# Optimization experiments

Hardware: AMD Instinct MI355X
Metric: run time of the kernel (lower is better)

Reference implementation:

```python
import jax, jax.numpy as jnp
import numpy as np

EPS = 1e-5  # BatchNorm1d default eps
NUM_HEADS = 8


def repbn(x, alpha, gamma, beta, rm, rv):
    # eval-mode RepBN over the channel (last) dim: BN(running stats) + alpha * x
    bn = (x - rm) * (gamma / jnp.sqrt(rv + EPS)) + beta
    return bn + alpha * x


def _forward(x, W_qkv, b_qkv, W_proj, b_proj, W1, b1, W2, b2, sa_w, sa_b,
             alpha1, gamma1, beta1, rm1, rv1, alpha2, gamma2, beta2, rm2, rv2):
    B, C, H, W = x.shape
    N = H * W
    D = C // NUM_HEADS
    t = x.reshape(B, C, N).transpose(0, 2, 1)  # [B, N, C]
    # --- FlashAttention (manual MHSA) ---
    qkv = (t @ W_qkv + b_qkv).reshape(B, N, 3, NUM_HEADS, D)
    q = qkv[:, :, 0].transpose(0, 2, 1, 3)  # [B, h, N, D]
    k = qkv[:, :, 1].transpose(0, 2, 1, 3)
    v = qkv[:, :, 2].transpose(0, 2, 1, 3)
    attn = jax.nn.softmax(jnp.einsum('bhnd,bhmd->bhnm', q, k) * (D ** -0.5), axis=-1)
    o = jnp.einsum('bhnm,bhmd->bhnd', attn, v).transpose(0, 2, 1, 3).reshape(B, N, C)
    o = o @ W_proj + b_proj
    # residual + blended norm (eval -> RepBN)
    t = repbn(t + o, alpha1, gamma1, beta1, rm1, rv1)
    # --- FFN with SpatialSILU activation ---
    h = t @ W1 + b1  # [B, N, cm]
    # depthwise 1x1 conv over the batch dim (channels==B per original unsqueeze(0))
    wgt = sa_w[:, None, None] * h + sa_b[:, None, None]
    h = h * jax.nn.sigmoid(wgt * h)
    f = h @ W2 + b2
    t = repbn(t + f, alpha2, gamma2, beta2, rm2, rv2)
    return t.transpose(0, 2, 1).reshape(B, C, H, W)


def setup_inputs() -> dict:
    key = jax.random.key(0)
    ks = jax.random.split(key, 8)
    B, C, H, W = 256, 256, 14, 14
    cm = 2048
    s = 0.02
    f32 = jnp.float32
    return {
        'x': jax.random.normal(ks[0], (B, C, H, W), f32),
        'W_qkv': jax.random.normal(ks[1], (C, 3 * C), f32) * s,
        'b_qkv': jnp.zeros((3 * C,), f32),
        'W_proj': jax.random.normal(ks[2], (C, C), f32) * s,
        'b_proj': jnp.zeros((C,), f32),
        'W1': jax.random.normal(ks[3], (C, cm), f32) * s,
        'b1': jnp.zeros((cm,), f32),
        'W2': jax.random.normal(ks[4], (cm, C), f32) * s,
        'b2': jnp.zeros((C,), f32),
        'sa_w': jax.random.normal(ks[5], (B,), f32) * s,
        'sa_b': jnp.zeros((B,), f32),
        'alpha1': jnp.ones((), f32),
        'gamma1': jnp.ones((C,), f32),
        'beta1': jnp.zeros((C,), f32),
        'rm1': jax.random.normal(ks[6], (C,), f32) * 0.1,
        'rv1': jnp.ones((C,), f32),
        'alpha2': jnp.ones((), f32),
        'gamma2': jnp.ones((C,), f32),
        'beta2': jnp.zeros((C,), f32),
        'rm2': jax.random.normal(ks[7], (C,), f32) * 0.1,
        'rv2': jnp.ones((C,), f32),
    }


def reference(x, W_qkv, b_qkv, W_proj, b_proj, W1, b1, W2, b2, sa_w, sa_b,
              alpha1, gamma1, beta1, rm1, rv1, alpha2, gamma2, beta2, rm2, rv2):
    return _forward(x, W_qkv, b_qkv, W_proj, b_proj, W1, b1, W2, b2, sa_w, sa_b,
                    alpha1, gamma1, beta1, rm1, rv1, alpha2, gamma2, beta2, rm2, rv2)
```

## Files before the change

kernel.cpp:

```cpp
#include <hip/hip_runtime.h>

using u16 = unsigned short;

typedef __bf16 bf16x8 __attribute__((ext_vector_type(8)));
typedef u16    u16x8  __attribute__((ext_vector_type(8)));
typedef float  f32x4  __attribute__((ext_vector_type(4)));

__device__ __forceinline__ float b2f(u16 u) {
    union { unsigned int i; float f; } c; c.i = ((unsigned int)u) << 16; return c.f;
}
__device__ __forceinline__ u16 f2b(float f) {
    union { float f; unsigned int i; } c; c.f = f;
    unsigned int i = c.i;
    return (u16)((i + 0x7FFFu + ((i >> 16) & 1u)) >> 16);
}
__device__ __forceinline__ float u2f(unsigned int u) {
    union { unsigned int i; float f; } c; c.i = u; return c.f;
}

#define AS1 __attribute__((address_space(1)))
#define AS3 __attribute__((address_space(3)))
__device__ __forceinline__ void glds16(const u16* g, u16* l) {
    __builtin_amdgcn_global_load_lds((const AS1 void*)(const void*)g,
                                     (AS3 void*)(void*)l, 16, 0, 0);
}

__global__ void btrans_f2b(const float* __restrict__ in, u16* __restrict__ out, int R, int C) {
    __shared__ u16 tile[32][33];
    const int c0 = blockIdx.x * 32, r0 = blockIdx.y * 32;
    const size_t base = (size_t)blockIdx.z * R * C;
    const int tx = threadIdx.x, ty = threadIdx.y;
    #pragma unroll
    for (int i = ty; i < 32; i += 8) {
        int r = r0 + i, c = c0 + tx;
        tile[i][tx] = (r < R && c < C) ? f2b(in[base + (size_t)r * C + c]) : (u16)0;
    }
    __syncthreads();
    #pragma unroll
    for (int i = ty; i < 32; i += 8) {
        int c = c0 + i, r = r0 + tx;
        if (c < C && r < R) out[base + (size_t)c * R + r] = tile[tx][i];
    }
}

__global__ void btrans_b2f(const u16* __restrict__ in, float* __restrict__ out, int R, int C) {
    __shared__ u16 tile[32][33];
    const int c0 = blockIdx.x * 32, r0 = blockIdx.y * 32;
    const size_t base = (size_t)blockIdx.z * R * C;
    const int tx = threadIdx.x, ty = threadIdx.y;
    #pragma unroll
    for (int i = ty; i < 32; i += 8) {
        int r = r0 + i, c = c0 + tx;
        tile[i][tx] = (r < R && c < C) ? in[base + (size_t)r * C + c] : (u16)0;
    }
    __syncthreads();
    #pragma unroll
    for (int i = ty; i < 32; i += 8) {
        int c = c0 + i, r = r0 + tx;
        if (c < C && r < R) out[base + (size_t)c * R + r] = b2f(tile[tx][i]);
    }
}

template<int EPI>
__launch_bounds__(512, 4)
__global__ void gemm_bt(const u16* __restrict__ A, const u16* __restrict__ BT,
                        const float* __restrict__ bias, u16* __restrict__ C,
                        int M, int N, int K, int row0,
                        const u16* __restrict__ R0,
                        const float* __restrict__ g, const float* __restrict__ be,
                        const float* __restrict__ rmv, const float* __restrict__ rvv,
                        const float* __restrict__ alpha,
                        const float* __restrict__ saw, const float* __restrict__ sab) {
    __shared__ __align__(16) u16 SL[16384];
    const int tid  = threadIdx.x;
    const int wave = tid >> 6, lane = tid & 63;
    const int wm = wave >> 2, wn = wave & 3;
    const int quad = lane >> 4, l16 = lane & 15;

    const unsigned gx = gridDim.x;
    unsigned lin = blockIdx.y * gx + blockIdx.x;
    const unsigned nwg = gx * gridDim.y;
    const unsigned q8 = nwg >> 3, r8 = nwg & 7;
    const unsigned xcd = lin & 7, loc = lin >> 3;
    lin = (xcd < r8 ? xcd * (q8 + 1) : r8 * (q8 + 1) + (xcd - r8) * q8) + loc;
    const int m0 = (int)(lin / gx) * 128, n0 = (int)(lin % gx) * 128;

    const int srow = lane >> 2;
    const int scol = (((lane & 3) ^ ((srow >> 1) & 3)) * 8);
    const size_t aoff = (size_t)(m0 + wave * 16 + srow) * K + scol;
    const size_t boff = (size_t)(n0 + wave * 16 + srow) * K + scol;
    u16* aS = SL + wave * 512;
    u16* bS = SL + 8192 + wave * 512;

    const int cfrag = (quad ^ ((l16 >> 1) & 3)) * 8;

    f32x4 acc[4][2] = {};
    const int niter = K >> 5;

    auto stage = [&](int buf, size_t kn) {
        const int bo = buf * 4096;
        glds16(A  + aoff + kn, aS + bo);
        glds16(BT + boff + kn, bS + bo);
    };

    auto kstep = [&](int cur, int kt) {
        __syncthreads();
        if (kt + 1 < niter) stage(cur ^ 1, (size_t)(kt + 1) << 5);
        const u16* ab = SL + cur * 4096;
        const u16* bb = SL + 8192 + cur * 4096;
        bf16x8 af[4], bfr[2];
        #pragma unroll
        for (int i = 0; i < 4; i++)
            af[i] = *(const bf16x8*)&ab[(wm * 64 + i * 16 + l16) * 32 + cfrag];
        #pragma unroll
        for (int j = 0; j < 2; j++)
            bfr[j] = *(const bf16x8*)&bb[(wn * 32 + j * 16 + l16) * 32 + cfrag];
        #pragma unroll
        for (int i = 0; i < 4; i++)
            #pragma unroll
            for (int j = 0; j < 2; j++)
                acc[i][j] = __builtin_amdgcn_mfma_f32_16x16x32_bf16(af[i], bfr[j], acc[i][j], 0, 0, 0);
    };

    stage(0, 0);
    int kt = 0;
    for (; kt + 2 <= niter; kt += 2) { kstep(0, kt); kstep(1, kt + 1); }
    if (kt < niter) kstep(kt & 1, kt);

    __syncthreads();

    float alphav = 0.f;
    if (EPI == 1) alphav = alpha[0];

    if (EPI == 1) {
        #pragma unroll
        for (int c = tid; c < 2048; c += 512) {
            int row = c >> 4, colc = (c & 15) * 8;
            *(u16x8*)&SL[row * 128 + colc] =
                *(const u16x8*)&R0[(size_t)(m0 + row) * N + n0 + colc];
        }
        __syncthreads();
    }

    float biasv[2], k0v[2], k1v[2];
    #pragma unroll
    for (int j = 0; j < 2; j++) {
        const int col = n0 + wn * 32 + j * 16 + l16;
        biasv[j] = bias[col];
        if (EPI == 1) {
            float sc = g[col] * rsqrtf(rvv[col] + 1e-5f);
            k1v[j] = sc + alphav;
            k0v[j] = be[col] - rmv[col] * sc;
        }
    }

    const int dup = l16 & 1;
    const int pr  = l16 >> 1;
    u16* Crow = C + (size_t)(m0 + wm * 64 + quad * 4 + 2 * dup) * N
                  + (n0 + wn * 32 + pr * 2);

    #pragma unroll
    for (int i = 0; i < 4; i++) {
        #pragma unroll
        for (int j = 0; j < 2; j++) {
            float vv[4];
            #pragma unroll
            for (int r = 0; r < 4; r++) {
                float v = acc[i][j][r] + biasv[j];
                if (EPI == 1) {
                    const int rowL = wm * 64 + i * 16 + quad * 4 + r;
                    const int colp = wn * 32 + j * 16 + (l16 & ~1);
                    unsigned rd = *(const unsigned*)&SL[rowL * 128 + colp];
                    unsigned fb = dup ? (rd & 0xffff0000u) : (rd << 16);
                    float x = v + u2f(fb);
                    v = fmaf(x, k1v[j], k0v[j]);
                } else if (EPI == 2) {
                    const int row = row0 + m0 + wm * 64 + i * 16 + quad * 4 + r;
                    const int bidx = row / 196;
                    float w = fmaf(saw[bidx], v, sab[bidx]);
                    v = v / (1.f + __expf(-w * v));
                }
                vv[r] = v;
            }
            unsigned D[4];
            #pragma unroll
            for (int r = 0; r < 4; r++) {
                float o  = __shfl_xor(vv[r], 1, 64);
                float lo = dup ? o : vv[r];
                float hi = dup ? vv[r] : o;
                unsigned d;
                asm("v_cvt_pk_bf16_f32 %0, %1, %2" : "=v"(d) : "v"(lo), "v"(hi));
                D[r] = d;
            }
            unsigned s0 = dup ? D[2] : D[0];
            unsigned s1 = dup ? D[3] : D[1];
            u16* p = Crow + (size_t)i * 16 * N + j * 16;
            *(unsigned*)p       = s0;
            *(unsigned*)(p + N) = s1;
        }
    }
}

__launch_bounds__(256)
__global__ void attn_kernel(const u16* __restrict__ qkv, u16* __restrict__ o) {
    __shared__ __align__(16) u16 Kb[224 * 32];
    __shared__ __align__(16) u16 Vt[32 * 232];
    __shared__ __align__(16) u16 Pl[4][16 * 232];
    const int tid  = threadIdx.x;
    const int wave = tid >> 6, lane = tid & 63;
    const int quad = lane >> 4, l16 = lane & 15;
    const int b = blockIdx.x >> 3, h = blockIdx.x & 7;
    const u16* qg = qkv + (size_t)b * 196 * 768 + h * 32;
    const float scale = 0.17677669529663687f;

    for (int idx = tid; idx < 896; idx += 256) {
        int row = idx >> 2, dp = (idx & 3) * 8;
        u16x8 kv = {};
        if (row < 196) kv = *(const u16x8*)&qg[(size_t)row * 768 + 256 + dp];
        *(u16x8*)&Kb[row * 32 + dp] = kv;
    }
    for (int idx = tid; idx < 224 * 32; idx += 256) {
        int row = idx >> 5, d = idx & 31;
        Vt[d * 232 + row] = (row < 196) ? qg[(size_t)row * 768 + 512 + d] : (u16)0;
    }
    for (int c = lane; c < 16 * 24; c += 64) {
        int m = c / 24, cc = 208 + (c % 24);
        Pl[wave][m * 232 + cc] = 0;
    }
    __syncthreads();

    for (int t = wave; t < 13; t += 4) {
        const int m0 = t * 16;
        bf16x8 aq = {};
        const int qrow = m0 + l16;
        if (qrow < 196) aq = *(const bf16x8*)&qg[(size_t)qrow * 768 + quad * 8];

        f32x4 s[13];
        #pragma unroll
        for (int ct = 0; ct < 13; ct++) {
            bf16x8 bk = *(const bf16x8*)&Kb[(ct * 16 + l16) * 32 + quad * 8];
            s[ct] = __builtin_amdgcn_mfma_f32_16x16x32_bf16(aq, bk, (f32x4){0.f, 0.f, 0.f, 0.f}, 0, 0, 0);
        }
        if (l16 >= 4) {
            #pragma unroll
            for (int r = 0; r < 4; r++) s[12][r] = -1e30f;
        }
        float mx[4] = {-1e30f, -1e30f, -1e30f, -1e30f};
        #pragma unroll
        for (int ct = 0; ct < 13; ct++)
            #pragma unroll
            for (int r = 0; r < 4; r++) mx[r] = fmaxf(mx[r], s[ct][r]);
        #pragma unroll
        for (int off = 1; off < 16; off <<= 1)
            #pragma unroll
            for (int r = 0; r < 4; r++) mx[r] = fmaxf(mx[r], __shfl_xor(mx[r], off, 64));
        float sum[4] = {0.f, 0.f, 0.f, 0.f};
        #pragma unroll
        for (int ct = 0; ct < 13; ct++) {
            #pragma unroll
            for (int r = 0; r < 4; r++) {
                float p = __expf((s[ct][r] - mx[r]) * scale);
                sum[r] += p;
                Pl[wave][(quad * 4 + r) * 232 + ct * 16 + l16] = f2b(p);
            }
        }
        #pragma unroll
        for (int off = 1; off < 16; off <<= 1)
            #pragma unroll
            for (int r = 0; r < 4; r++) sum[r] += __shfl_xor(sum[r], off, 64);
        float inv[4];
        #pragma unroll
        for (int r = 0; r < 4; r++) inv[r] = 1.f / sum[r];

        #pragma unroll
        for (int nt = 0; nt < 2; nt++) {
            f32x4 ao = {0.f, 0.f, 0.f, 0.f};
            #pragma unroll
            for (int kc = 0; kc < 7; kc++) {
                bf16x8 ap = *(const bf16x8*)&Pl[wave][l16 * 232 + kc * 32 + quad * 8];
                bf16x8 bv = *(const bf16x8*)&Vt[(nt * 16 + l16) * 232 + kc * 32 + quad * 8];
                ao = __builtin_amdgcn_mfma_f32_16x16x32_bf16(ap, bv, ao, 0, 0, 0);
            }
            #pragma unroll
            for (int r = 0; r < 4; r++) {
                const int gm = m0 + quad * 4 + r;
                if (gm < 196)
                    o[((size_t)b * 196 + gm) * 256 + h * 32 + nt * 16 + l16] = f2b(ao[r] * inv[r]);
            }
        }
    }
}

extern "C" void kernel_launch(void* const* d_in, const int* in_sizes, int n_in,
                              void* d_out, int out_size, void* d_ws, size_t ws_size,
                              hipStream_t stream) {
    const float* x      = (const float*)d_in[0];
    const float* Wqkv   = (const float*)d_in[1];
    const float* bqkv   = (const float*)d_in[2];
    const float* Wproj  = (const float*)d_in[3];
    const float* bproj  = (const float*)d_in[4];
    const float* W1     = (const float*)d_in[5];
    const float* b1     = (const float*)d_in[6];
    const float* W2     = (const float*)d_in[7];
    const float* b2     = (const float*)d_in[8];
    const float* saw    = (const float*)d_in[9];
    const float* sab    = (const float*)d_in[10];
    const float* alpha1 = (const float*)d_in[11];
    const float* g1     = (const float*)d_in[12];
    const float* be1    = (const float*)d_in[13];
    const float* rm1    = (const float*)d_in[14];
    const float* rv1    = (const float*)d_in[15];
    const float* alpha2 = (const float*)d_in[16];
    const float* g2     = (const float*)d_in[17];
    const float* be2    = (const float*)d_in[18];
    const float* rm2    = (const float*)d_in[19];
    const float* rv2    = (const float*)d_in[20];

    const int B = 256, Cc = 256, Np = 196, CM = 2048;
    const int M = B * Np;

    auto al = [](size_t s) { return (s + 255) & ~(size_t)255; };
    char* ws = (char*)d_ws;
    const size_t o_t0  = 0;
    const size_t o_t1  = o_t0 + al((size_t)M * Cc * 2);
    const size_t o_wq  = o_t1 + al((size_t)M * Cc * 2);
    const size_t o_wp  = o_wq + al((size_t)768 * Cc * 2);
    const size_t o_w1  = o_wp + al((size_t)Cc * Cc * 2);
    const size_t o_w2  = o_w1 + al((size_t)Cc * CM * 2);
    const size_t o_scr = o_w2 + al((size_t)CM * Cc * 2);
    const size_t S = (ws_size > o_scr) ? ws_size - o_scr : 0;

    u16* t0     = (u16*)(ws + o_t0);
    u16* t1b    = (u16*)(ws + o_t1);
    u16* WqkvT  = (u16*)(ws + o_wq);
    u16* WprojT = (u16*)(ws + o_wp);
    u16* W1T    = (u16*)(ws + o_w1);
    u16* W2T    = (u16*)(ws + o_w2);
    u16* scr    = (u16*)(ws + o_scr);
    u16* t2     = t0;
    u16* obuf   = (u16*)d_out;
    float* out  = (float*)d_out;

    int nq = 1; while (nq < 8 && ((size_t)(M / nq) * 768 * 2) > S) nq *= 2;
    const int nf_opts[7] = {1, 2, 4, 8, 14, 28, 56};
    int nf = 56;
    for (int i = 0; i < 7; ++i) {
        if (((size_t)(M / nf_opts[i]) * CM * 2) <= S) { nf = nf_opts[i]; break; }
    }
    const int Mq = M / nq, Bq = B / nq;
    const int Mf = M / nf;

    dim3 tb(32, 8, 1);
    btrans_f2b<<<dim3((Np + 31) / 32, (Cc + 31) / 32, B), tb, 0, stream>>>(x, t0, Cc, Np);
    btrans_f2b<<<dim3(768 / 32, Cc / 32, 1), tb, 0, stream>>>(Wqkv,  WqkvT,  Cc, 768);
    btrans_f2b<<<dim3(Cc  / 32, Cc / 32, 1), tb, 0, stream>>>(Wproj, WprojT, Cc, Cc);
    btrans_f2b<<<dim3(CM  / 32, Cc / 32, 1), tb, 0, stream>>>(W1,    W1T,    Cc, CM);
    btrans_f2b<<<dim3(Cc  / 32, CM / 32, 1), tb, 0, stream>>>(W2,    W2T,    CM, Cc);

    for (int c = 0; c < nq; ++c) {
        gemm_bt<0><<<dim3(768 / 128, Mq / 128), 512, 0, stream>>>(
            t0 + (size_t)c * Mq * Cc, WqkvT, bqkv, scr, Mq, 768, Cc, 0,
            nullptr, nullptr, nullptr, nullptr, nullptr, nullptr, nullptr, nullptr);
        attn_kernel<<<dim3(Bq * 8), 256, 0, stream>>>(scr, obuf + (size_t)c * Mq * Cc);
    }

    gemm_bt<1><<<dim3(Cc / 128, M / 128), 512, 0, stream>>>(
        obuf, WprojT, bproj, t1b, M, Cc, Cc, 0,
        t0, g1, be1, rm1, rv1, alpha1, nullptr, nullptr);

    for (int c = 0; c < nf; ++c) {
        gemm_bt<2><<<dim3(CM / 128, Mf / 128), 512, 0, stream>>>(
            t1b + (size_t)c * Mf * Cc, W1T, b1, scr, Mf, CM, Cc, c * Mf,
            nullptr, nullptr, nullptr, nullptr, nullptr, nullptr, saw, sab);
        gemm_bt<1><<<dim3(Cc / 128, Mf / 128), 512, 0, stream>>>(
            scr, W2T, b2, t2 + (size_t)c * Mf * Cc, Mf, Cc, CM, 0,
            t1b + (size_t)c * Mf * Cc, g2, be2, rm2, rv2, alpha2, nullptr, nullptr);
    }

    btrans_b2f<<<dim3((Cc + 31) / 32, (Np + 31) / 32, B), tb, 0, stream>>>(t2, out, Np, Cc);
}
```

Measured before the change: 542.9 us.

## Enlarge GEMM block tile to 256x128 with 64x64 per-wave tiles

Changes the GEMM block tile from 128x128 to 256x128. The 8 waves are rearranged into a 4x2 grid, so each wave owns a 64x64 output tile and accumulates 4x4 MFMA fragments. The aim is more data reuse per LDS fragment load and less global traffic per output. In exchange the LDS footprint, accumulator register pressure and residual-epilogue complexity all grow: the residual is now staged in two halves with extra barriers. The grid shrinks to half as many blocks, and chunking options are trimmed so the row counts stay divisible by 256, which may reduce occupancy and parallelism.

```diff
diff --git a/kernel.cpp b/kernel.cpp
--- a/kernel.cpp
+++ b/kernel.cpp
@@ -71,10 +71,10 @@
                         const float* __restrict__ rmv, const float* __restrict__ rvv,
                         const float* __restrict__ alpha,
                         const float* __restrict__ saw, const float* __restrict__ sab) {
-    __shared__ __align__(16) u16 SL[16384];
+    __shared__ __align__(16) u16 SL[24576];
     const int tid  = threadIdx.x;
     const int wave = tid >> 6, lane = tid & 63;
-    const int wm = wave >> 2, wn = wave & 3;
+    const int wm = wave >> 1, wn = wave & 1;
     const int quad = lane >> 4, l16 = lane & 15;
 
     const unsigned gx = gridDim.x;
@@ -83,42 +83,41 @@
     const unsigned q8 = nwg >> 3, r8 = nwg & 7;
     const unsigned xcd = lin & 7, loc = lin >> 3;
     lin = (xcd < r8 ? xcd * (q8 + 1) : r8 * (q8 + 1) + (xcd - r8) * q8) + loc;
-    const int m0 = (int)(lin / gx) * 128, n0 = (int)(lin % gx) * 128;
+    const int m0 = (int)(lin / gx) * 256, n0 = (int)(lin % gx) * 128;
 
     const int srow = lane >> 2;
     const int scol = (((lane & 3) ^ ((srow >> 1) & 3)) * 8);
-    const size_t aoff = (size_t)(m0 + wave * 16 + srow) * K + scol;
-    const size_t boff = (size_t)(n0 + wave * 16 + srow) * K + scol;
-    u16* aS = SL + wave * 512;
-    u16* bS = SL + 8192 + wave * 512;
+    const size_t aoff0 = (size_t)(m0 + wave * 32 + srow) * K + scol;
+    const size_t aoff1 = aoff0 + (size_t)16 * K;
+    const size_t boff  = (size_t)(n0 + wave * 16 + srow) * K + scol;
 
     const int cfrag = (quad ^ ((l16 >> 1) & 3)) * 8;
 
-    f32x4 acc[4][2] = {};
+    f32x4 acc[4][4] = {};
     const int niter = K >> 5;
 
     auto stage = [&](int buf, size_t kn) {
-        const int bo = buf * 4096;
-        glds16(A  + aoff + kn, aS + bo);
-        glds16(BT + boff + kn, bS + bo);
+        glds16(A  + aoff0 + kn, SL + buf * 8192 + wave * 1024);
+        glds16(A  + aoff1 + kn, SL + buf * 8192 + wave * 1024 + 512);
+        glds16(BT + boff  + kn, SL + 16384 + buf * 4096 + wave * 512);
     };
 
     auto kstep = [&](int cur, int kt) {
         __syncthreads();
         if (kt + 1 < niter) stage(cur ^ 1, (size_t)(kt + 1) << 5);
-        const u16* ab = SL + cur * 4096;
-        const u16* bb = SL + 8192 + cur * 4096;
-        bf16x8 af[4], bfr[2];
+        const u16* ab = SL + cur * 8192;
+        const u16* bb = SL + 16384 + cur * 4096;
+        bf16x8 af[4], bfr[4];
         #pragma unroll
         for (int i = 0; i < 4; i++)
             af[i] = *(const bf16x8*)&ab[(wm * 64 + i * 16 + l16) * 32 + cfrag];
         #pragma unroll
-        for (int j = 0; j < 2; j++)
-            bfr[j] = *(const bf16x8*)&bb[(wn * 32 + j * 16 + l16) * 32 + cfrag];
+        for (int j = 0; j < 4; j++)
+            bfr[j] = *(const bf16x8*)&bb[(wn * 64 + j * 16 + l16) * 32 + cfrag];
         #pragma unroll
         for (int i = 0; i < 4; i++)
             #pragma unroll
-            for (int j = 0; j < 2; j++)
+            for (int j = 0; j < 4; j++)
                 acc[i][j] = __builtin_amdgcn_mfma_f32_16x16x32_bf16(af[i], bfr[j], acc[i][j], 0, 0, 0);
     };
 
@@ -132,20 +131,10 @@
     float alphav = 0.f;
     if (EPI == 1) alphav = alpha[0];
 
-    if (EPI == 1) {
-        #pragma unroll
-        for (int c = tid; c < 2048; c += 512) {
-            int row = c >> 4, colc = (c & 15) * 8;
-            *(u16x8*)&SL[row * 128 + colc] =
-                *(const u16x8*)&R0[(size_t)(m0 + row) * N + n0 + colc];
-        }
-        __syncthreads();
-    }
-
-    float biasv[2], k0v[2], k1v[2];
-    #pragma unroll
-    for (int j = 0; j < 2; j++) {
-        const int col = n0 + wn * 32 + j * 16 + l16;
+    float biasv[4], k0v[4], k1v[4];
+    #pragma unroll
+    for (int j = 0; j < 4; j++) {
+        const int col = n0 + wn * 64 + j * 16 + l16;
         biasv[j] = bias[col];
         if (EPI == 1) {
             float sc = g[col] * rsqrtf(rvv[col] + 1e-5f);
@@ -157,47 +146,72 @@
     const int dup = l16 & 1;
     const int pr  = l16 >> 1;
     u16* Crow = C + (size_t)(m0 + wm * 64 + quad * 4 + 2 * dup) * N
-                  + (n0 + wn * 32 + pr * 2);
-
-    #pragma unroll
-    for (int i = 0; i < 4; i++) {
-        #pragma unroll
-        for (int j = 0; j < 2; j++) {
-            float vv[4];
-            #pragma unroll
-            for (int r = 0; r < 4; r++) {
-                float v = acc[i][j][r] + biasv[j];
-                if (EPI == 1) {
-                    const int rowL = wm * 64 + i * 16 + quad * 4 + r;
-                    const int colp = wn * 32 + j * 16 + (l16 & ~1);
-                    unsigned rd = *(const unsigned*)&SL[rowL * 128 + colp];
-                    unsigned fb = dup ? (rd & 0xffff0000u) : (rd << 16);
-                    float x = v + u2f(fb);
-                    v = fmaf(x, k1v[j], k0v[j]);
-                } else if (EPI == 2) {
+                  + (n0 + wn * 64 + pr * 2);
+
+    auto emit = [&]() {
+        #pragma unroll
+        for (int i = 0; i < 4; i++) {
+            float swv4[4], sbv4[4];
+            if (EPI == 2) {
+                #pragma unroll
+                for (int r = 0; r < 4; r++) {
                     const int row = row0 + m0 + wm * 64 + i * 16 + quad * 4 + r;
                     const int bidx = row / 196;
-                    float w = fmaf(saw[bidx], v, sab[bidx]);
-                    v = v / (1.f + __expf(-w * v));
+                    swv4[r] = saw[bidx]; sbv4[r] = sab[bidx];
                 }
-                vv[r] = v;
-            }
-            unsigned D[4];
-            #pragma unroll
-            for (int r = 0; r < 4; r++) {
-                float o  = __shfl_xor(vv[r], 1, 64);
-                float lo = dup ? o : vv[r];
-                float hi = dup ? vv[r] : o;
-                unsigned d;
-                asm("v_cvt_pk_bf16_f32 %0, %1, %2" : "=v"(d) : "v"(lo), "v"(hi));
-                D[r] = d;
-            }
-            unsigned s0 = dup ? D[2] : D[0];
-            unsigned s1 = dup ? D[3] : D[1];
-            u16* p = Crow + (size_t)i * 16 * N + j * 16;
-            *(unsigned*)p       = s0;
-            *(unsigned*)(p + N) = s1;
-        }
+            }
+            #pragma unroll
+            for (int j = 0; j < 4; j++) {
+                float vv[4];
+                #pragma unroll
+                for (int r = 0; r < 4; r++) {
+                    float v = acc[i][j][r] + biasv[j];
+                    if (EPI == 1) {
+                        const int rowL = (wm & 1) * 64 + i * 16 + quad * 4 + r;
+                        const int colp = wn * 64 + j * 16 + (l16 & ~1);
+                        unsigned rd = *(const unsigned*)&SL[rowL * 128 + colp];
+                        unsigned fb = dup ? (rd & 0xffff0000u) : (rd << 16);
+                        float x = v + u2f(fb);
+                        v = fmaf(x, k1v[j], k0v[j]);
+                    } else if (EPI == 2) {
+                        float w = fmaf(swv4[r], v, sbv4[r]);
+                        v = v / (1.f + __expf(-w * v));
+                    }
+                    vv[r] = v;
+                }
+                unsigned D[4];
+                #pragma unroll
+                for (int r = 0; r < 4; r++) {
+                    float o  = __shfl_xor(vv[r], 1, 64);
+                    float lo = dup ? o : vv[r];
+                    float hi = dup ? vv[r] : o;
+                    unsigned d;
+                    asm("v_cvt_pk_bf16_f32 %0, %1, %2" : "=v"(d) : "v"(lo), "v"(hi));
+                    D[r] = d;
+                }
+                unsigned s0 = dup ? D[2] : D[0];
+                unsigned s1 = dup ? D[3] : D[1];
+                u16* p = Crow + (size_t)i * 16 * N + j * 16;
+                *(unsigned*)p       = s0;
+                *(unsigned*)(p + N) = s1;
+            }
+        }
+    };
+
+    if (EPI == 1) {
+        #pragma unroll
+        for (int h = 0; h < 2; h++) {
+            for (int c = tid; c < 2048; c += 512) {
+                int row = c >> 4, colc = (c & 15) * 8;
+                *(u16x8*)&SL[row * 128 + colc] =
+                    *(const u16x8*)&R0[(size_t)(m0 + h * 128 + row) * N + n0 + colc];
+            }
+            __syncthreads();
+            if ((wm >> 1) == h) emit();
+            __syncthreads();
+        }
+    } else {
+        emit();
     }
 }
 
@@ -341,10 +355,10 @@
     u16* obuf   = (u16*)d_out;
     float* out  = (float*)d_out;
 
-    int nq = 1; while (nq < 8 && ((size_t)(M / nq) * 768 * 2) > S) nq *= 2;
-    const int nf_opts[7] = {1, 2, 4, 8, 14, 28, 56};
+    int nq = 1; while (nq < 4 && ((size_t)(M / nq) * 768 * 2) > S) nq *= 2;
+    const int nf_opts[6] = {1, 2, 4, 14, 28, 56};
     int nf = 56;
-    for (int i = 0; i < 7; ++i) {
+    for (int i = 0; i < 6; ++i) {
         if (((size_t)(M / nf_opts[i]) * CM * 2) <= S) { nf = nf_opts[i]; break; }
     }
     const int Mq = M / nq, Bq = B / nq;
@@ -358,21 +372,21 @@
     btrans_f2b<<<dim3(Cc  / 32, CM / 32, 1), tb, 0, stream>>>(W2,    W2T,    CM, Cc);
 
     for (int c = 0; c < nq; ++c) {
-        gemm_bt<0><<<dim3(768 / 128, Mq / 128), 512, 0, stream>>>(
+        gemm_bt<0><<<dim3(768 / 128, Mq / 256), 512, 0, stream>>>(
             t0 + (size_t)c * Mq * Cc, WqkvT, bqkv, scr, Mq, 768, Cc, 0,
             nullptr, nullptr, nullptr, nullptr, nullptr, nullptr, nullptr, nullptr);
         attn_kernel<<<dim3(Bq * 8), 256, 0, stream>>>(scr, obuf + (size_t)c * Mq * Cc);
     }
 
-    gemm_bt<1><<<dim3(Cc / 128, M / 128), 512, 0, stream>>>(
+    gemm_bt<1><<<dim3(Cc / 128, M / 256), 512, 0, stream>>>(
         obuf, WprojT, bproj, t1b, M, Cc, Cc, 0,
         t0, g1, be1, rm1, rv1, alpha1, nullptr, nullptr);
 
     for (int c = 0; c < nf; ++c) {
-        gemm_bt<2><<<dim3(CM / 128, Mf / 128), 512, 0, stream>>>(
+        gemm_bt<2><<<dim3(CM / 128, Mf / 256), 512, 0, stream>>>(
             t1b + (size_t)c * Mf * Cc, W1T, b1, scr, Mf, CM, Cc, c * Mf,
             nullptr, nullptr, nullptr, nullptr, nullptr, nullptr, saw, sab);
-        gemm_bt<1><<<dim3(Cc / 128, Mf / 128), 512, 0, stream>>>(
+        gemm_bt<1><<<dim3(Cc / 128, Mf / 256), 512, 0, stream>>>(
             scr, W2T, b2, t2 + (size_t)c * Mf * Cc, Mf, Cc, CM, 0,
             t1b + (size_t)c * Mf * Cc, g2, be2, rm2, rv2, alpha2, nullptr, nullptr);
     }
```

After: 526.2 us. -3.1%, faster.
